# Kernel tuning notes

Measured on AMD Instinct MI355X. Metric: run time of the kernel, lower is better.

## Reference

```python
import jax, jax.numpy as jnp
import numpy as np

AFWD = 0.999
EPS = 1e-05


def setup_inputs() -> dict:
    key = jax.random.key(0)
    N, L = 8192, 4096
    x = jax.random.normal(key, (N, L), dtype=jnp.float32)
    m = jnp.zeros((L,), dtype=jnp.float32)    # EMA mean buffer (init 0)
    var = jnp.ones((L,), dtype=jnp.float32)   # EMA var buffer (init 1)
    return {"x": x, "m": m, "var": var}


def reference(x, m, var):
    """Online-normalization forward: sequential scan over the N (row) dim,
    vectorized over the L feature dim. Matches ControlNormalization.forward."""
    afwd = AFWD

    def step(carry, xt):
        mu, v = carry                      # each [L]
        scale = jnp.sqrt(v + EPS)
        d = xt - mu
        out = d / scale
        v_new = afwd * v + afwd * (1.0 - afwd) * d * d
        mu_new = mu + (1.0 - afwd) * d
        return (mu_new, v_new), out

    _, out = jax.lax.scan(step, (m, var), x)  # out: [N, L]
    return out
```

## Files before the change

kernel.cpp:

```cpp
#include <hip/hip_runtime.h>
#include <math.h>

#define AFWD 0.999f
#define ONE_MINUS_A (1.0f - 0.999f)
#define KCOEF (0.999f * (1.0f - 0.999f))
#define EPSV 1e-5f

typedef float floatx4 __attribute__((ext_vector_type(4)));

__global__ __launch_bounds__(256) void
passA(const float* __restrict__ x, float* __restrict__ Bmu,
      float* __restrict__ See, float* __restrict__ Te, int L4, int CH) {
  int idx  = blockIdx.x * blockDim.x + threadIdx.x;
  int col4 = idx % L4;
  int c    = idx / L4;
  const floatx4* xv = (const floatx4*)x;
  int base = c * CH * L4 + col4;

  float mu[4] = {0.f, 0.f, 0.f, 0.f};
  float s[4]  = {0.f, 0.f, 0.f, 0.f};
  float t[4]  = {0.f, 0.f, 0.f, 0.f};

#pragma unroll 4
  for (int i = 0; i < CH; ++i) {
    floatx4 v = xv[base + i * L4];
#pragma unroll
    for (int k = 0; k < 4; ++k) {
      float e = v[k] - mu[k];
      s[k] = fmaf(AFWD, s[k], e * e);
      t[k] += e;
      mu[k] = fmaf(ONE_MINUS_A, e, mu[k]);
    }
  }

  int o = c * L4 + col4;
  floatx4 om = {mu[0], mu[1], mu[2], mu[3]};
  floatx4 os = {s[0], s[1], s[2], s[3]};
  floatx4 ot = {t[0], t[1], t[2], t[3]};
  ((floatx4*)Bmu)[o] = om;
  ((floatx4*)See)[o] = os;
  ((floatx4*)Te)[o]  = ot;
}

__device__ __forceinline__ float
weighted_scan_incl(float u, float A, int c, int C, float* sm) {
  float p = u;
  float w = A;
  for (int off = 1; off < C; off <<= 1) {
    __syncthreads();
    sm[c] = p;
    __syncthreads();
    if (c >= off) p = fmaf(w, sm[c - off], p);
    w *= w;
  }
  return p;
}

__global__ void
passB_scan(const float* __restrict__ m, const float* __restrict__ var,
           const float* __restrict__ Bmu, const float* __restrict__ See,
           const float* __restrict__ Te, float* __restrict__ Ms,
           float* __restrict__ Vs, int L, int C, float A, float c_eg,
           float Sgg) {
  extern __shared__ float sm[];
  int l = blockIdx.x;
  int c = threadIdx.x;
  int o = c * L + l;

  float bmu = Bmu[o];
  float see = See[o];
  float te  = Te[o];
  float M0 = m[l];
  float V0 = var[l];

  float Ac = 1.0f, Ap = A;
#pragma unroll
  for (int b = 0; b < 10; ++b) {
    if (c & (1 << b)) Ac *= Ap;
    Ap *= Ap;
  }

  float p = weighted_scan_incl(bmu, A, c, C, sm);
  __syncthreads();
  sm[c] = p;
  __syncthreads();
  float M = fmaf(Ac, M0, (c > 0) ? sm[c - 1] : 0.0f);

  float w = KCOEF * fmaf(M * M, Sgg, fmaf(-2.0f * c_eg * M, te, see));
  float q = weighted_scan_incl(w, A, c, C, sm);
  __syncthreads();
  sm[c] = q;
  __syncthreads();
  float V = fmaf(Ac, V0, (c > 0) ? sm[c - 1] : 0.0f);

  Ms[o] = M;
  Vs[o] = V;
}

__global__ __launch_bounds__(256) void
passC(const float* __restrict__ x, const float* __restrict__ Ms,
      const float* __restrict__ Vs, float* __restrict__ out, int L4, int CH) {
  int idx  = blockIdx.x * blockDim.x + threadIdx.x;
  int col4 = idx % L4;
  int c    = idx / L4;
  const floatx4* xv = (const floatx4*)x;
  floatx4* ov = (floatx4*)out;
  int base = c * CH * L4 + col4;

  int o = c * L4 + col4;
  floatx4 m4 = ((const floatx4*)Ms)[o];
  floatx4 v4 = ((const floatx4*)Vs)[o];
  float mu[4] = {m4[0], m4[1], m4[2], m4[3]};
  float vv[4] = {v4[0], v4[1], v4[2], v4[3]};

#pragma unroll 4
  for (int i = 0; i < CH; ++i) {
    floatx4 v = xv[base + i * L4];
    floatx4 oe;
#pragma unroll
    for (int k = 0; k < 4; ++k) {
      float d = v[k] - mu[k];
      oe[k] = d * rsqrtf(vv[k] + EPSV);
      vv[k] = fmaf(AFWD, vv[k], KCOEF * (d * d));
      mu[k] = fmaf(ONE_MINUS_A, d, mu[k]);
    }
    __builtin_nontemporal_store(oe, &ov[base + i * L4]);
  }
}

extern "C" void kernel_launch(void* const* d_in, const int* in_sizes, int n_in,
                              void* d_out, int out_size, void* d_ws, size_t ws_size,
                              hipStream_t stream) {
  const float* x   = (const float*)d_in[0];
  const float* m   = (const float*)d_in[1];
  const float* var = (const float*)d_in[2];
  float* out = (float*)d_out;

  int L  = in_sizes[1];
  int N  = in_sizes[0] / L;
  int L4 = L / 4;

  int C = 128;
  while (C > 1 && ((size_t)5 * C * L * sizeof(float) > ws_size || (N % C) != 0))
    C >>= 1;
  int CH = N / C;

  double a = 0.999;
  float A    = (float)pow(a, (double)CH);
  float c_eg = (float)pow(a, (double)(CH - 1));
  float Sgg  = (float)(pow(a, (double)(CH - 1)) * (1.0 - pow(a, (double)CH)) / (1.0 - a));

  float* ws  = (float*)d_ws;
  size_t CL  = (size_t)C * L;
  float* Bmu = ws;
  float* See = ws + CL;
  float* Te  = ws + 2 * CL;
  float* Ms  = ws + 3 * CL;
  float* Vs  = ws + 4 * CL;

  int threadsBig = C * L4;
  passA<<<threadsBig / 256, 256, 0, stream>>>(x, Bmu, See, Te, L4, CH);
  passB_scan<<<L, C, C * sizeof(float), stream>>>(m, var, Bmu, See, Te, Ms, Vs,
                                                  L, C, A, c_eg, Sgg);
  passC<<<threadsBig / 256, 256, 0, stream>>>(x, Ms, Vs, out, L4, CH);
}
```

Before: 92.43 us.

## Fuse three passes into one cooperative kernel with grid syncs

Merges the chunk-summary pass, the cross-chunk scan pass and the output pass into a single cooperative kernel separated by grid-wide barriers. The scan phase is redistributed so each workgroup handles several columns with subgroups of C threads. This is meant to remove the launch overhead and gaps between kernels. In exchange it adds grid sync costs and reduces the parallelism of the scan phase, and it requires the whole grid to be co-resident.

```diff
diff --git a/kernel.cpp b/kernel.cpp
--- a/kernel.cpp
+++ b/kernel.cpp
@@ -1,5 +1,8 @@
 #include <hip/hip_runtime.h>
+#include <hip/hip_cooperative_groups.h>
 #include <math.h>
+
+namespace cg = cooperative_groups;
 
 #define AFWD 0.999f
 #define ONE_MINUS_A (1.0f - 0.999f)
@@ -9,122 +12,116 @@
 typedef float floatx4 __attribute__((ext_vector_type(4)));
 
 __global__ __launch_bounds__(256) void
-passA(const float* __restrict__ x, float* __restrict__ Bmu,
-      float* __restrict__ See, float* __restrict__ Te, int L4, int CH) {
+fused_cn(const float* __restrict__ x, const float* __restrict__ m,
+         const float* __restrict__ var, float* __restrict__ out,
+         float* __restrict__ Bmu, float* __restrict__ See,
+         float* __restrict__ Te, float* __restrict__ Ms,
+         float* __restrict__ Vs, int L, int L4, int C, int CH,
+         float A, float c_eg, float Sgg) {
+  cg::grid_group grid = cg::this_grid();
+  __shared__ float sm[2 * (256 + 8)];
+
   int idx  = blockIdx.x * blockDim.x + threadIdx.x;
   int col4 = idx % L4;
   int c    = idx / L4;
   const floatx4* xv = (const floatx4*)x;
   int base = c * CH * L4 + col4;
+  int o    = c * L4 + col4;
 
-  float mu[4] = {0.f, 0.f, 0.f, 0.f};
-  float s[4]  = {0.f, 0.f, 0.f, 0.f};
-  float t[4]  = {0.f, 0.f, 0.f, 0.f};
+  {
+    float mu[4] = {0.f, 0.f, 0.f, 0.f};
+    float s[4]  = {0.f, 0.f, 0.f, 0.f};
+    float t[4]  = {0.f, 0.f, 0.f, 0.f};
+#pragma unroll 4
+    for (int i = 0; i < CH; ++i) {
+      floatx4 v = xv[base + i * L4];
+#pragma unroll
+      for (int k = 0; k < 4; ++k) {
+        float e = v[k] - mu[k];
+        s[k] = fmaf(AFWD, s[k], e * e);
+        t[k] += e;
+        mu[k] = fmaf(ONE_MINUS_A, e, mu[k]);
+      }
+    }
+    floatx4 om = {mu[0], mu[1], mu[2], mu[3]};
+    floatx4 os = {s[0], s[1], s[2], s[3]};
+    floatx4 ot = {t[0], t[1], t[2], t[3]};
+    ((floatx4*)Bmu)[o] = om;
+    ((floatx4*)See)[o] = os;
+    ((floatx4*)Te)[o]  = ot;
+  }
 
-#pragma unroll 4
-  for (int i = 0; i < CH; ++i) {
-    floatx4 v = xv[base + i * L4];
+  grid.sync();
+
+  {
+    int nWG       = gridDim.x;
+    int colsPerWG = L / nWG;
+    int groups    = blockDim.x / C;
+    int sub       = threadIdx.x / C;
+    int cc        = threadIdx.x % C;
+    float* smb = &sm[sub * (C + 8)];
+
+    float Ac = 1.0f, Ap = A;
 #pragma unroll
-    for (int k = 0; k < 4; ++k) {
-      float e = v[k] - mu[k];
-      s[k] = fmaf(AFWD, s[k], e * e);
-      t[k] += e;
-      mu[k] = fmaf(ONE_MINUS_A, e, mu[k]);
+    for (int b = 0; b < 8; ++b) {
+      if (cc & (1 << b)) Ac *= Ap;
+      Ap *= Ap;
+    }
+
+    for (int j = 0; j < colsPerWG; j += groups) {
+      int l  = blockIdx.x * colsPerWG + j + sub;
+      int oo = cc * L + l;
+      float bmu = Bmu[oo];
+      float see = See[oo];
+      float te  = Te[oo];
+      float M0  = m[l];
+      float V0  = var[l];
+
+      float p = bmu, w = A;
+      for (int off = 1; off < C; off <<= 1) {
+        __syncthreads(); smb[cc] = p; __syncthreads();
+        if (cc >= off) p = fmaf(w, smb[cc - off], p);
+        w *= w;
+      }
+      __syncthreads(); smb[cc] = p; __syncthreads();
+      float M = fmaf(Ac, M0, cc ? smb[cc - 1] : 0.0f);
+
+      float wv = KCOEF * fmaf(M * M, Sgg, fmaf(-2.0f * c_eg * M, te, see));
+      float q = wv; w = A;
+      for (int off = 1; off < C; off <<= 1) {
+        __syncthreads(); smb[cc] = q; __syncthreads();
+        if (cc >= off) q = fmaf(w, smb[cc - off], q);
+        w *= w;
+      }
+      __syncthreads(); smb[cc] = q; __syncthreads();
+      float V = fmaf(Ac, V0, cc ? smb[cc - 1] : 0.0f);
+
+      Ms[oo] = M;
+      Vs[oo] = V;
     }
   }
 
-  int o = c * L4 + col4;
-  floatx4 om = {mu[0], mu[1], mu[2], mu[3]};
-  floatx4 os = {s[0], s[1], s[2], s[3]};
-  floatx4 ot = {t[0], t[1], t[2], t[3]};
-  ((floatx4*)Bmu)[o] = om;
-  ((floatx4*)See)[o] = os;
-  ((floatx4*)Te)[o]  = ot;
-}
+  grid.sync();
 
-__device__ __forceinline__ float
-weighted_scan_incl(float u, float A, int c, int C, float* sm) {
-  float p = u;
-  float w = A;
-  for (int off = 1; off < C; off <<= 1) {
-    __syncthreads();
-    sm[c] = p;
-    __syncthreads();
-    if (c >= off) p = fmaf(w, sm[c - off], p);
-    w *= w;
-  }
-  return p;
-}
-
-__global__ void
-passB_scan(const float* __restrict__ m, const float* __restrict__ var,
-           const float* __restrict__ Bmu, const float* __restrict__ See,
-           const float* __restrict__ Te, float* __restrict__ Ms,
-           float* __restrict__ Vs, int L, int C, float A, float c_eg,
-           float Sgg) {
-  extern __shared__ float sm[];
-  int l = blockIdx.x;
-  int c = threadIdx.x;
-  int o = c * L + l;
-
-  float bmu = Bmu[o];
-  float see = See[o];
-  float te  = Te[o];
-  float M0 = m[l];
-  float V0 = var[l];
-
-  float Ac = 1.0f, Ap = A;
+  {
+    floatx4* ov = (floatx4*)out;
+    floatx4 m4 = ((const floatx4*)Ms)[o];
+    floatx4 v4 = ((const floatx4*)Vs)[o];
+    float mu[4] = {m4[0], m4[1], m4[2], m4[3]};
+    float vv[4] = {v4[0], v4[1], v4[2], v4[3]};
+#pragma unroll 4
+    for (int i = 0; i < CH; ++i) {
+      floatx4 v = xv[base + i * L4];
+      floatx4 oe;
 #pragma unroll
-  for (int b = 0; b < 10; ++b) {
-    if (c & (1 << b)) Ac *= Ap;
-    Ap *= Ap;
-  }
-
-  float p = weighted_scan_incl(bmu, A, c, C, sm);
-  __syncthreads();
-  sm[c] = p;
-  __syncthreads();
-  float M = fmaf(Ac, M0, (c > 0) ? sm[c - 1] : 0.0f);
-
-  float w = KCOEF * fmaf(M * M, Sgg, fmaf(-2.0f * c_eg * M, te, see));
-  float q = weighted_scan_incl(w, A, c, C, sm);
-  __syncthreads();
-  sm[c] = q;
-  __syncthreads();
-  float V = fmaf(Ac, V0, (c > 0) ? sm[c - 1] : 0.0f);
-
-  Ms[o] = M;
-  Vs[o] = V;
-}
-
-__global__ __launch_bounds__(256) void
-passC(const float* __restrict__ x, const float* __restrict__ Ms,
-      const float* __restrict__ Vs, float* __restrict__ out, int L4, int CH) {
-  int idx  = blockIdx.x * blockDim.x + threadIdx.x;
-  int col4 = idx % L4;
-  int c    = idx / L4;
-  const floatx4* xv = (const floatx4*)x;
-  floatx4* ov = (floatx4*)out;
-  int base = c * CH * L4 + col4;
-
-  int o = c * L4 + col4;
-  floatx4 m4 = ((const floatx4*)Ms)[o];
-  floatx4 v4 = ((const floatx4*)Vs)[o];
-  float mu[4] = {m4[0], m4[1], m4[2], m4[3]};
-  float vv[4] = {v4[0], v4[1], v4[2], v4[3]};
-
-#pragma unroll 4
-  for (int i = 0; i < CH; ++i) {
-    floatx4 v = xv[base + i * L4];
-    floatx4 oe;
-#pragma unroll
-    for (int k = 0; k < 4; ++k) {
-      float d = v[k] - mu[k];
-      oe[k] = d * rsqrtf(vv[k] + EPSV);
-      vv[k] = fmaf(AFWD, vv[k], KCOEF * (d * d));
-      mu[k] = fmaf(ONE_MINUS_A, d, mu[k]);
+      for (int k = 0; k < 4; ++k) {
+        float d = v[k] - mu[k];
+        oe[k] = d * rsqrtf(vv[k] + EPSV);
+        vv[k] = fmaf(AFWD, vv[k], KCOEF * (d * d));
+        mu[k] = fmaf(ONE_MINUS_A, d, mu[k]);
+      }
+      __builtin_nontemporal_store(oe, &ov[base + i * L4]);
     }
-    __builtin_nontemporal_store(oe, &ov[base + i * L4]);
   }
 }
 
@@ -159,8 +156,11 @@
   float* Vs  = ws + 4 * CL;
 
   int threadsBig = C * L4;
-  passA<<<threadsBig / 256, 256, 0, stream>>>(x, Bmu, See, Te, L4, CH);
-  passB_scan<<<L, C, C * sizeof(float), stream>>>(m, var, Bmu, See, Te, Ms, Vs,
-                                                  L, C, A, c_eg, Sgg);
-  passC<<<threadsBig / 256, 256, 0, stream>>>(x, Ms, Vs, out, L4, CH);
+  dim3 grid(threadsBig / 256), block(256);
+  void* args[] = {(void*)&x,   (void*)&m,   (void*)&var, (void*)&out,
+                  (void*)&Bmu, (void*)&See, (void*)&Te,  (void*)&Ms,
+                  (void*)&Vs,  (void*)&L,   (void*)&L4,  (void*)&C,
+                  (void*)&CH,  (void*)&A,   (void*)&c_eg, (void*)&Sgg};
+  hipLaunchCooperativeKernel((const void*)fused_cn, grid, block, args, 0,
+                             stream);
 }
```

After: 221.7 us. +139.9%, slower.

## Double scan chunk count and manually batch four row loads per iteration

Applied to the files above, without the earlier changes.

Raises the number of row chunks from 128 to 256, which doubles the threads in the sequential passes and halves each thread's serial chain length. The inner loops of pass A and pass C are manually unrolled to issue four independent vector loads before the dependent arithmetic, and the four stores are grouped at the end. The scan helper is inlined by hand. The trade-off is a larger workspace and a longer block-level scan in pass B (256 threads, more sync steps). The chunk-size check now requires chunk length divisible by 4.

```diff
diff --git a/kernel.cpp b/kernel.cpp
--- a/kernel.cpp
+++ b/kernel.cpp
@@ -21,14 +21,34 @@
   float s[4]  = {0.f, 0.f, 0.f, 0.f};
   float t[4]  = {0.f, 0.f, 0.f, 0.f};
 
-#pragma unroll 4
-  for (int i = 0; i < CH; ++i) {
-    floatx4 v = xv[base + i * L4];
-#pragma unroll
-    for (int k = 0; k < 4; ++k) {
-      float e = v[k] - mu[k];
-      s[k] = fmaf(AFWD, s[k], e * e);
-      t[k] += e;
+#pragma unroll 1
+  for (int i = 0; i < CH; i += 4) {
+    floatx4 v0 = xv[base + (i + 0) * L4];
+    floatx4 v1 = xv[base + (i + 1) * L4];
+    floatx4 v2 = xv[base + (i + 2) * L4];
+    floatx4 v3 = xv[base + (i + 3) * L4];
+#pragma unroll
+    for (int k = 0; k < 4; ++k) {
+      float e = v0[k] - mu[k];
+      s[k] = fmaf(AFWD, s[k], e * e); t[k] += e;
+      mu[k] = fmaf(ONE_MINUS_A, e, mu[k]);
+    }
+#pragma unroll
+    for (int k = 0; k < 4; ++k) {
+      float e = v1[k] - mu[k];
+      s[k] = fmaf(AFWD, s[k], e * e); t[k] += e;
+      mu[k] = fmaf(ONE_MINUS_A, e, mu[k]);
+    }
+#pragma unroll
+    for (int k = 0; k < 4; ++k) {
+      float e = v2[k] - mu[k];
+      s[k] = fmaf(AFWD, s[k], e * e); t[k] += e;
+      mu[k] = fmaf(ONE_MINUS_A, e, mu[k]);
+    }
+#pragma unroll
+    for (int k = 0; k < 4; ++k) {
+      float e = v3[k] - mu[k];
+      s[k] = fmaf(AFWD, s[k], e * e); t[k] += e;
       mu[k] = fmaf(ONE_MINUS_A, e, mu[k]);
     }
   }
@@ -40,20 +60,6 @@
   ((floatx4*)Bmu)[o] = om;
   ((floatx4*)See)[o] = os;
   ((floatx4*)Te)[o]  = ot;
-}
-
-__device__ __forceinline__ float
-weighted_scan_incl(float u, float A, int c, int C, float* sm) {
-  float p = u;
-  float w = A;
-  for (int off = 1; off < C; off <<= 1) {
-    __syncthreads();
-    sm[c] = p;
-    __syncthreads();
-    if (c >= off) p = fmaf(w, sm[c - off], p);
-    w *= w;
-  }
-  return p;
 }
 
 __global__ void
@@ -80,18 +86,24 @@
     Ap *= Ap;
   }
 
-  float p = weighted_scan_incl(bmu, A, c, C, sm);
-  __syncthreads();
-  sm[c] = p;
-  __syncthreads();
-  float M = fmaf(Ac, M0, (c > 0) ? sm[c - 1] : 0.0f);
-
-  float w = KCOEF * fmaf(M * M, Sgg, fmaf(-2.0f * c_eg * M, te, see));
-  float q = weighted_scan_incl(w, A, c, C, sm);
-  __syncthreads();
-  sm[c] = q;
-  __syncthreads();
-  float V = fmaf(Ac, V0, (c > 0) ? sm[c - 1] : 0.0f);
+  float p = bmu, w = A;
+  for (int off = 1; off < C; off <<= 1) {
+    __syncthreads(); sm[c] = p; __syncthreads();
+    if (c >= off) p = fmaf(w, sm[c - off], p);
+    w *= w;
+  }
+  __syncthreads(); sm[c] = p; __syncthreads();
+  float M = fmaf(Ac, M0, c ? sm[c - 1] : 0.0f);
+
+  float wv = KCOEF * fmaf(M * M, Sgg, fmaf(-2.0f * c_eg * M, te, see));
+  float q = wv; w = A;
+  for (int off = 1; off < C; off <<= 1) {
+    __syncthreads(); sm[c] = q; __syncthreads();
+    if (c >= off) q = fmaf(w, sm[c - off], q);
+    w *= w;
+  }
+  __syncthreads(); sm[c] = q; __syncthreads();
+  float V = fmaf(Ac, V0, c ? sm[c - 1] : 0.0f);
 
   Ms[o] = M;
   Vs[o] = V;
@@ -113,18 +125,45 @@
   float mu[4] = {m4[0], m4[1], m4[2], m4[3]};
   float vv[4] = {v4[0], v4[1], v4[2], v4[3]};
 
-#pragma unroll 4
-  for (int i = 0; i < CH; ++i) {
-    floatx4 v = xv[base + i * L4];
-    floatx4 oe;
-#pragma unroll
-    for (int k = 0; k < 4; ++k) {
-      float d = v[k] - mu[k];
-      oe[k] = d * rsqrtf(vv[k] + EPSV);
-      vv[k] = fmaf(AFWD, vv[k], KCOEF * (d * d));
-      mu[k] = fmaf(ONE_MINUS_A, d, mu[k]);
-    }
-    __builtin_nontemporal_store(oe, &ov[base + i * L4]);
+#pragma unroll 1
+  for (int i = 0; i < CH; i += 4) {
+    floatx4 v0 = xv[base + (i + 0) * L4];
+    floatx4 v1 = xv[base + (i + 1) * L4];
+    floatx4 v2 = xv[base + (i + 2) * L4];
+    floatx4 v3 = xv[base + (i + 3) * L4];
+    floatx4 o0, o1, o2, o3;
+#pragma unroll
+    for (int k = 0; k < 4; ++k) {
+      float d = v0[k] - mu[k];
+      o0[k] = d * rsqrtf(vv[k] + EPSV);
+      vv[k] = fmaf(AFWD, vv[k], KCOEF * (d * d));
+      mu[k] = fmaf(ONE_MINUS_A, d, mu[k]);
+    }
+#pragma unroll
+    for (int k = 0; k < 4; ++k) {
+      float d = v1[k] - mu[k];
+      o1[k] = d * rsqrtf(vv[k] + EPSV);
+      vv[k] = fmaf(AFWD, vv[k], KCOEF * (d * d));
+      mu[k] = fmaf(ONE_MINUS_A, d, mu[k]);
+    }
+#pragma unroll
+    for (int k = 0; k < 4; ++k) {
+      float d = v2[k] - mu[k];
+      o2[k] = d * rsqrtf(vv[k] + EPSV);
+      vv[k] = fmaf(AFWD, vv[k], KCOEF * (d * d));
+      mu[k] = fmaf(ONE_MINUS_A, d, mu[k]);
+    }
+#pragma unroll
+    for (int k = 0; k < 4; ++k) {
+      float d = v3[k] - mu[k];
+      o3[k] = d * rsqrtf(vv[k] + EPSV);
+      vv[k] = fmaf(AFWD, vv[k], KCOEF * (d * d));
+      mu[k] = fmaf(ONE_MINUS_A, d, mu[k]);
+    }
+    __builtin_nontemporal_store(o0, &ov[base + (i + 0) * L4]);
+    __builtin_nontemporal_store(o1, &ov[base + (i + 1) * L4]);
+    __builtin_nontemporal_store(o2, &ov[base + (i + 2) * L4]);
+    __builtin_nontemporal_store(o3, &ov[base + (i + 3) * L4]);
   }
 }
 
@@ -140,8 +179,9 @@
   int N  = in_sizes[0] / L;
   int L4 = L / 4;
 
-  int C = 128;
-  while (C > 1 && ((size_t)5 * C * L * sizeof(float) > ws_size || (N % C) != 0))
+  int C = 256;
+  while (C > 1 && ((size_t)5 * C * L * sizeof(float) > ws_size ||
+                   (N % C) != 0 || (N / C) % 4 != 0))
     C >>= 1;
   int CH = N / C;
 
```

Result: slower. 103.4 us (+11.9%).

## Replace shared-memory chunk scan with hierarchical three-level sequential scan

Applied to the files above, without the earlier changes.

The per-feature block-wide weighted Hillis-Steele scan, which needed many __syncthreads and strided one-float-per-thread loads, is replaced by three kernels. The first combines groups of 16 chunk summaries into super-chunk summaries, the second scans those sequentially per feature, and the third rescans within each group to produce per-chunk starting mean and variance. The intent is to remove barrier-heavy scan steps and get coalesced loads across the feature dimension. In exchange it adds two extra kernel launches and extra workspace traffic, and the composed summary algebra could change rounding slightly.

```diff
diff --git a/kernel.cpp b/kernel.cpp
--- a/kernel.cpp
+++ b/kernel.cpp
@@ -42,59 +42,81 @@
   ((floatx4*)Te)[o]  = ot;
 }
 
-__device__ __forceinline__ float
-weighted_scan_incl(float u, float A, int c, int C, float* sm) {
-  float p = u;
-  float w = A;
-  for (int off = 1; off < C; off <<= 1) {
-    __syncthreads();
-    sm[c] = p;
-    __syncthreads();
-    if (c >= off) p = fmaf(w, sm[c - off], p);
-    w *= w;
-  }
-  return p;
-}
-
-__global__ void
-passB_scan(const float* __restrict__ m, const float* __restrict__ var,
-           const float* __restrict__ Bmu, const float* __restrict__ See,
-           const float* __restrict__ Te, float* __restrict__ Ms,
-           float* __restrict__ Vs, int L, int C, float A, float c_eg,
-           float Sgg) {
-  extern __shared__ float sm[];
-  int l = blockIdx.x;
-  int c = threadIdx.x;
-  int o = c * L + l;
-
-  float bmu = Bmu[o];
-  float see = See[o];
-  float te  = Te[o];
-  float M0 = m[l];
-  float V0 = var[l];
-
-  float Ac = 1.0f, Ap = A;
-#pragma unroll
-  for (int b = 0; b < 10; ++b) {
-    if (c & (1 << b)) Ac *= Ap;
-    Ap *= Ap;
-  }
-
-  float p = weighted_scan_incl(bmu, A, c, C, sm);
-  __syncthreads();
-  sm[c] = p;
-  __syncthreads();
-  float M = fmaf(Ac, M0, (c > 0) ? sm[c - 1] : 0.0f);
-
-  float w = KCOEF * fmaf(M * M, Sgg, fmaf(-2.0f * c_eg * M, te, see));
-  float q = weighted_scan_incl(w, A, c, C, sm);
-  __syncthreads();
-  sm[c] = q;
-  __syncthreads();
-  float V = fmaf(Ac, V0, (c > 0) ? sm[c - 1] : 0.0f);
-
-  Ms[o] = M;
-  Vs[o] = V;
+__global__ __launch_bounds__(256) void
+passB1(const float* __restrict__ Bmu, const float* __restrict__ See,
+       const float* __restrict__ Te, float* __restrict__ Bsup,
+       float* __restrict__ Ssup, float* __restrict__ Tsup, int L, int SUB,
+       float A, float c_eg, float Sgg, float G) {
+  int idx = blockIdx.x * blockDim.x + threadIdx.x;
+  int l   = idx % L;
+  int g   = idx / L;
+  int base = g * SUB * L + l;
+
+  float B = 0.f, T = 0.f, S = 0.f;
+#pragma unroll 16
+  for (int k = 0; k < SUB; ++k) {
+    int o = base + k * L;
+    float b2 = Bmu[o];
+    float s2 = See[o];
+    float t2 = Te[o];
+    S = fmaf(A, S, fmaf(Sgg * B, B, fmaf(-2.0f * c_eg * B, t2, s2)));
+    T = fmaf(-G, B, T + t2);
+    B = fmaf(A, B, b2);
+  }
+  int o = g * L + l;
+  Bsup[o] = B;
+  Ssup[o] = S;
+  Tsup[o] = T;
+}
+
+__global__ __launch_bounds__(256) void
+passB2(const float* __restrict__ m, const float* __restrict__ var,
+       const float* __restrict__ Bsup, const float* __restrict__ Ssup,
+       const float* __restrict__ Tsup, float* __restrict__ Mg,
+       float* __restrict__ Vg, int L, int GS, float Asup, float c_sup,
+       float Sggsup) {
+  int l = blockIdx.x * blockDim.x + threadIdx.x;
+  float M = m[l];
+  float V = var[l];
+#pragma unroll 8
+  for (int g = 0; g < GS; ++g) {
+    int o = g * L + l;
+    Mg[o] = M;
+    Vg[o] = V;
+    float b = Bsup[o];
+    float s = Ssup[o];
+    float t = Tsup[o];
+    float sum = fmaf(M * M, Sggsup, fmaf(-2.0f * c_sup * M, t, s));
+    V = fmaf(Asup, V, KCOEF * sum);
+    M = fmaf(Asup, M, b);
+  }
+}
+
+__global__ __launch_bounds__(256) void
+passB3(const float* __restrict__ Bmu, const float* __restrict__ See,
+       const float* __restrict__ Te, const float* __restrict__ Mg,
+       const float* __restrict__ Vg, float* __restrict__ Ms,
+       float* __restrict__ Vs, int L, int SUB, float A, float c_eg,
+       float Sgg) {
+  int idx = blockIdx.x * blockDim.x + threadIdx.x;
+  int l   = idx % L;
+  int g   = idx / L;
+  int base = g * SUB * L + l;
+
+  float M = Mg[g * L + l];
+  float V = Vg[g * L + l];
+#pragma unroll 16
+  for (int k = 0; k < SUB; ++k) {
+    int o = base + k * L;
+    Ms[o] = M;
+    Vs[o] = V;
+    float b = Bmu[o];
+    float s = See[o];
+    float t = Te[o];
+    float sum = fmaf(M * M, Sgg, fmaf(-2.0f * c_eg * M, t, s));
+    V = fmaf(A, V, KCOEF * sum);
+    M = fmaf(A, M, b);
+  }
 }
 
 __global__ __launch_bounds__(256) void
@@ -141,26 +163,44 @@
   int L4 = L / 4;
 
   int C = 128;
-  while (C > 1 && ((size_t)5 * C * L * sizeof(float) > ws_size || (N % C) != 0))
+  while (C > 1 && ((size_t)(5 * C + 5 * (C / 16 + 1)) * L * sizeof(float) > ws_size ||
+                   (N % C) != 0))
     C >>= 1;
   int CH = N / C;
+  int SUB = (C >= 16) ? 16 : C;
+  int GS  = C / SUB;
 
   double a = 0.999;
   float A    = (float)pow(a, (double)CH);
   float c_eg = (float)pow(a, (double)(CH - 1));
   float Sgg  = (float)(pow(a, (double)(CH - 1)) * (1.0 - pow(a, (double)CH)) / (1.0 - a));
+  float G    = (float)((1.0 - pow(a, (double)CH)) / (1.0 - a));
+  double nS = (double)SUB * CH;
+  float Asup   = (float)pow(a, nS);
+  float c_sup  = (float)pow(a, nS - 1.0);
+  float Sggsup = (float)(pow(a, nS - 1.0) * (1.0 - pow(a, nS)) / (1.0 - a));
 
   float* ws  = (float*)d_ws;
   size_t CL  = (size_t)C * L;
-  float* Bmu = ws;
-  float* See = ws + CL;
-  float* Te  = ws + 2 * CL;
-  float* Ms  = ws + 3 * CL;
-  float* Vs  = ws + 4 * CL;
+  size_t GL  = (size_t)GS * L;
+  float* Bmu  = ws;
+  float* See  = ws + CL;
+  float* Te   = ws + 2 * CL;
+  float* Ms   = ws + 3 * CL;
+  float* Vs   = ws + 4 * CL;
+  float* Bsup = ws + 5 * CL;
+  float* Ssup = Bsup + GL;
+  float* Tsup = Bsup + 2 * GL;
+  float* Mg   = Bsup + 3 * GL;
+  float* Vg   = Bsup + 4 * GL;
 
   int threadsBig = C * L4;
   passA<<<threadsBig / 256, 256, 0, stream>>>(x, Bmu, See, Te, L4, CH);
-  passB_scan<<<L, C, C * sizeof(float), stream>>>(m, var, Bmu, See, Te, Ms, Vs,
-                                                  L, C, A, c_eg, Sgg);
+  passB1<<<(L * GS) / 256, 256, 0, stream>>>(Bmu, See, Te, Bsup, Ssup, Tsup,
+                                             L, SUB, A, c_eg, Sgg, G);
+  passB2<<<L / 256, 256, 0, stream>>>(m, var, Bsup, Ssup, Tsup, Mg, Vg, L, GS,
+                                      Asup, c_sup, Sggsup);
+  passB3<<<(L * GS) / 256, 256, 0, stream>>>(Bmu, See, Te, Mg, Vg, Ms, Vs,
+                                             L, SUB, A, c_eg, Sgg);
   passC<<<threadsBig / 256, 256, 0, stream>>>(x, Ms, Vs, out, L4, CH);
 }
```

Result: faster. 85.26 us (-7.8%).
